# Kernel tuning notes

Measured on AMD Instinct MI355X. Metric: run time of the kernel, lower is better.

Reference implementation:

```python
import jax, jax.numpy as jnp
import numpy as np

B, S, H = 128, 1000, 256


def setup_inputs() -> dict:
    key = jax.random.key(0)
    ks = jax.random.split(key, 15)
    sc = 1.0 / np.sqrt(H)
    f = lambda k, shape: (jax.random.normal(k, shape, jnp.float32) * sc)
    return dict(
        static_hidden=jax.random.normal(ks[0], (B, S, H), jnp.float32),
        state_embedding=jax.random.normal(ks[1], (B, 1, H), jnp.float32),
        decoder_hidden=jax.random.normal(ks[2], (B, 1, H), jnp.float32),
        target_hidden=jax.random.normal(ks[3], (B, 1, H), jnp.float32),
        last_hh=jax.random.normal(ks[4], (1, B, H), jnp.float32),
        W_ih=f(ks[5], (3 * H, H)),
        W_hh=f(ks[6], (3 * H, H)),
        b_ih=f(ks[7], (3 * H,)),
        b_hh=f(ks[8], (3 * H,)),
        v_attn_enc=f(ks[9], (H,)),
        W_attn_enc=f(ks[10], (H, 2 * H)),
        v_attn_tgt=f(ks[11], (H,)),
        W_attn_tgt=f(ks[12], (H, 2 * H)),
        v_ptr=f(ks[13], (H,)),
        W_ptr=f(ks[14], (H, 3 * H)),
    )


def _attention(static, dec, v, W):
    # static: [B,S,H], dec: [B,1,H] -> softmax attention over S
    hid = jnp.concatenate([static, jnp.broadcast_to(dec, static.shape)], axis=2)  # [B,S,2H]
    t = jnp.tanh(jnp.einsum('hk,bsk->bhs', W, hid))  # [B,H,S]
    return jax.nn.softmax(jnp.einsum('h,bhs->bs', v, t), axis=1)  # [B,S]


def _gru_step(x, h, Wih, Whh, bih, bhh):
    # single-layer single-step torch GRU semantics; x,h: [B,H]
    gi = x @ Wih.T + bih
    gh = h @ Whh.T + bhh
    ir, iz, ig = jnp.split(gi, 3, axis=-1)
    hr, hz, hg = jnp.split(gh, 3, axis=-1)
    r = jax.nn.sigmoid(ir + hr)
    z = jax.nn.sigmoid(iz + hz)
    n = jnp.tanh(ig + r * hg)
    return (1.0 - z) * n + z * h


def _pointer_branch(static, state_emb, attn, v, W):
    context = jnp.einsum('bs,bsh->bh', attn, static)[:, None, :]  # [B,1,H]
    energy = jnp.concatenate(
        [static,
         jnp.broadcast_to(context, static.shape),
         jnp.broadcast_to(state_emb, static.shape)], axis=2)  # [B,S,3H]
    return jnp.einsum('h,bhs->bs', v, jnp.tanh(jnp.einsum('hk,bsk->bhs', W, energy)))


def reference(static_hidden, state_embedding, decoder_hidden, target_hidden, last_hh,
              W_ih, W_hh, b_ih, b_hh,
              v_attn_enc, W_attn_enc, v_attn_tgt, W_attn_tgt, v_ptr, W_ptr):
    # GRU step (dropout is identity in eval / p=0.0)
    h_new = _gru_step(decoder_hidden[:, 0, :], last_hh[0], W_ih, W_hh, b_ih, b_hh)
    rnn_out = h_new[:, None, :]  # [B,1,H]
    last_hh_new = h_new[None]    # [1,B,H]

    enc_attn = _attention(static_hidden, rnn_out, v_attn_enc, W_attn_enc)
    probs = _pointer_branch(static_hidden, state_embedding, enc_attn, v_ptr, W_ptr)

    tgt_attn = _attention(static_hidden, target_hidden, v_attn_tgt, W_attn_tgt)
    # NOTE: original code reuses self.v / self.W (not v_target/W_taret) for the
    # target branch energy -- replicated faithfully.
    probs_target = _pointer_branch(static_hidden, state_embedding, tgt_attn, v_ptr, W_ptr)

    return (5.0 * probs + probs_target, last_hh_new)
```

## Files before the change

### kernel.cpp

```cpp
#include <hip/hip_runtime.h>
#include <hip/hip_bf16.h>
#include <stdint.h>
#include <stddef.h>

#define Bn 128
#define Sn 1000
#define SP 1024
#define Hn 256

typedef __bf16 bf16;
typedef __bf16 bf16x8 __attribute__((ext_vector_type(8)));
typedef __bf16 bf16x4 __attribute__((ext_vector_type(4)));
typedef float  f32x16 __attribute__((ext_vector_type(16)));

typedef __attribute__((address_space(1))) const unsigned int* gas1;
typedef __attribute__((address_space(3))) unsigned int* las3;

__device__ __forceinline__ float fast_tanh(float x){
  return 1.0f - 2.0f / (__expf(2.0f * x) + 1.0f);
}
__device__ __forceinline__ float fast_sigmoid(float x){
  return 1.0f / (1.0f + __expf(-x));
}

__global__ void k0w(const float* __restrict__ We, const float* __restrict__ Wt,
                    const float* __restrict__ Wp, bf16* __restrict__ Wcb,
                    const float* __restrict__ dec, const float* __restrict__ lhh,
                    const float* __restrict__ tgt, const float* __restrict__ se,
                    float* __restrict__ xT, float* __restrict__ hT,
                    float* __restrict__ tT, float* __restrict__ sT){
  int blk = blockIdx.x, t = threadIdx.x;
  if (blk < 768){
    int tt = blk*256 + t;
    int r = tt >> 8, c = tt & 255;
    float val;
    if (r < 256)       val = We[r*512 + c];
    else if (r < 512)  val = Wt[(r-256)*512 + c];
    else               val = Wp[(r-512)*768 + c];
    Wcb[tt] = (bf16)val;
  } else {
    int idx = blk - 768;
    int a = idx >> 7, bb = idx & 127;
    const float* src = (a==0) ? dec : (a==1) ? lhh : (a==2) ? tgt : se;
    float* dst       = (a==0) ? xT  : (a==1) ? hT  : (a==2) ? tT  : sT;
    dst[t*128 + bb] = src[bb*256 + t];
  }
}

__global__ __launch_bounds__(512) void k1a_gru(
    const float* __restrict__ xT, const float* __restrict__ hT,
    const float* __restrict__ Wih, const float* __restrict__ Whh,
    const float* __restrict__ bih, const float* __restrict__ bhh,
    float* __restrict__ out_hh, float* __restrict__ hnT){
  int t = threadIdx.x;
  int g = t >> 7, b = t & 127;
  int h = blockIdx.x*4 + g;
  const float4* wir = (const float4*)(Wih + (size_t)h*256);
  const float4* wiz = (const float4*)(Wih + (size_t)(256+h)*256);
  const float4* wig = (const float4*)(Wih + (size_t)(512+h)*256);
  const float4* whr = (const float4*)(Whh + (size_t)h*256);
  const float4* whz = (const float4*)(Whh + (size_t)(256+h)*256);
  const float4* whg = (const float4*)(Whh + (size_t)(512+h)*256);
  float air=0.f, aiz=0.f, aig=0.f, ahr=0.f, ahz=0.f, ahg=0.f;
  #pragma unroll 2
  for (int kq=0; kq<64; kq++){
    float4 vir = wir[kq], viz = wiz[kq], vig = wig[kq];
    float4 vhr = whr[kq], vhz = whz[kq], vhg = whg[kq];
    #pragma unroll
    for (int e=0;e<4;e++){
      int k = kq*4 + e;
      float xv = xT[k*128 + b];
      float hv = hT[k*128 + b];
      air += (&vir.x)[e]*xv; aiz += (&viz.x)[e]*xv; aig += (&vig.x)[e]*xv;
      ahr += (&vhr.x)[e]*hv; ahz += (&vhz.x)[e]*hv; ahg += (&vhg.x)[e]*hv;
    }
  }
  air += bih[h];      ahr += bhh[h];
  aiz += bih[256+h];  ahz += bhh[256+h];
  aig += bih[512+h];  ahg += bhh[512+h];
  float r = fast_sigmoid(air + ahr);
  float z = fast_sigmoid(aiz + ahz);
  float n = fast_tanh(aig + r*ahg);
  float hprev = hT[h*128 + b];
  float hnew = (1.f - z)*n + z*hprev;
  out_hh[b*256 + h] = hnew;
  hnT[h*128 + b] = hnew;
}

__global__ __launch_bounds__(512) void k1c_dots(
    const float* __restrict__ hnT, const float* __restrict__ tT,
    const float* __restrict__ sT,
    const float* __restrict__ We, const float* __restrict__ Wt,
    const float* __restrict__ Wp,
    float* __restrict__ dEnc, float* __restrict__ dTgt, float* __restrict__ c3){
  int t = threadIdx.x;
  int g = t >> 7, b = t & 127;
  int vr = blockIdx.x*4 + g;
  int var = vr >> 8, h = vr & 255;
  const float* wrow; const float* X; float* dst;
  if (var == 0)      { wrow = We + (size_t)h*512 + 256; X = hnT; dst = dEnc; }
  else if (var == 1) { wrow = Wt + (size_t)h*512 + 256; X = tT;  dst = dTgt; }
  else               { wrow = Wp + (size_t)h*768 + 512; X = sT;  dst = c3; }
  const float4* w4 = (const float4*)wrow;
  float acc = 0.f;
  #pragma unroll 2
  for (int kq=0; kq<64; kq++){
    float4 wv = w4[kq];
    #pragma unroll
    for (int e=0;e<4;e++)
      acc += (&wv.x)[e] * X[(kq*4+e)*128 + b];
  }
  dst[b*256 + h] = acc;
}

__global__ __launch_bounds__(256) void k2_gemm(
    const float* __restrict__ stat, const bf16* __restrict__ Wcb,
    const float* __restrict__ dEnc, const float* __restrict__ dTgt,
    const float* __restrict__ vEnc, const float* __restrict__ vTgt,
    float* __restrict__ scE, float* __restrict__ scT, bf16* __restrict__ Aptr){
  __shared__ __align__(16) bf16 As[64*256];
  __shared__ __align__(16) bf16 Bs[2][256*32];
  int tid = threadIdx.x, w = tid>>6, l = tid&63;
  int l31 = l&31, lh = l>>5;
  int st = blockIdx.x, b = blockIdx.y;

  int am = tid>>2, agk = tid&3;
  bool aValid = (st*64 + am) < Sn;
  const float4* aSrc4 = (const float4*)(stat + ((size_t)b*Sn + st*64 + am)*Hn);

  int bnb = w*16 + (l>>2);
  int bg  = l&3;

  float4 pl0 = make_float4(0.f,0.f,0.f,0.f), pl1 = pl0;
  if (aValid){ pl0 = aSrc4[agk*2]; pl1 = aSrc4[agk*2+1]; }
  #pragma unroll
  for (int i=0;i<4;i++){
    int n = i*64 + bnb;
    int g = bg ^ ((n>>1)&3);
    __builtin_amdgcn_global_load_lds((gas1)(Wcb + (size_t)n*256 + g*8),
                                     (las3)(&Bs[0][i*2048 + w*512]), 16, 0, 0);
  }
  {
    bf16x8 v;
    v[0]=(bf16)pl0.x; v[1]=(bf16)pl0.y; v[2]=(bf16)pl0.z; v[3]=(bf16)pl0.w;
    v[4]=(bf16)pl1.x; v[5]=(bf16)pl1.y; v[6]=(bf16)pl1.z; v[7]=(bf16)pl1.w;
    *(bf16x8*)&As[am*256 + ((agk ^ (am&7))<<3)] = v;
  }
  __syncthreads();

  float scp0[2] = {0.f, 0.f}, scp1[2] = {0.f, 0.f};

  #pragma unroll
  for (int p=0; p<3; p++){
    f32x16 acc[2][2];
    #pragma unroll
    for (int a=0;a<2;a++)
      #pragma unroll
      for (int c=0;c<2;c++)
        #pragma unroll
        for (int r=0;r<16;r++) acc[a][c][r] = 0.f;

    #pragma unroll
    for (int kt=0; kt<8; kt++){
      int it = p*8 + kt;
      float4 q0 = make_float4(0.f,0.f,0.f,0.f), q1 = q0;
      bool doA = (p==0) && (kt<7);
      if (doA && aValid){ q0 = aSrc4[(kt+1)*8 + agk*2]; q1 = aSrc4[(kt+1)*8 + agk*2 + 1]; }
      if (it < 23){
        int itn = it+1, pn = itn>>3, ktn = itn&7;
        const bf16* wb = Wcb + (size_t)pn*65536 + ktn*32;
        bf16* ldsb = &Bs[(it&1)^1][0];
        #pragma unroll
        for (int i=0;i<4;i++){
          int n = i*64 + bnb;
          int g = bg ^ ((n>>1)&3);
          __builtin_amdgcn_global_load_lds((gas1)(wb + (size_t)n*256 + g*8),
                                           (las3)(ldsb + i*2048 + w*512), 16, 0, 0);
        }
      }
      const bf16* bsr = &Bs[it&1][0];
      #pragma unroll
      for (int ks=0; ks<2; ks++){
        int kg = ks*2 + lh;
        int swzA = ((kt*4 + kg) ^ (l31&7))<<3;
        bf16x8 af0 = *(const bf16x8*)&As[l31*256 + swzA];
        bf16x8 af1 = *(const bf16x8*)&As[(32+l31)*256 + swzA];
        #pragma unroll
        for (int c=0;c<2;c++){
          int n = w*64 + c*32 + l31;
          bf16x8 wf = *(const bf16x8*)&bsr[n*32 + ((kg ^ ((n>>1)&3))<<3)];
          acc[0][c] = __builtin_amdgcn_mfma_f32_32x32x16_bf16(wf, af0, acc[0][c], 0,0,0);
          acc[1][c] = __builtin_amdgcn_mfma_f32_32x32x16_bf16(wf, af1, acc[1][c], 0,0,0);
        }
      }
      if (doA){
        bf16x8 v;
        v[0]=(bf16)q0.x; v[1]=(bf16)q0.y; v[2]=(bf16)q0.z; v[3]=(bf16)q0.w;
        v[4]=(bf16)q1.x; v[5]=(bf16)q1.y; v[6]=(bf16)q1.z; v[7]=(bf16)q1.w;
        int G = (kt+1)*4 + agk;
        *(bf16x8*)&As[am*256 + ((G ^ (am&7))<<3)] = v;
      }
      __syncthreads();
    }

    if (p < 2){
      const float* vv = p ? vTgt : vEnc;
      const float* db = (p ? dTgt : dEnc) + b*256;
      float s0 = 0.f, s1 = 0.f;
      #pragma unroll
      for (int c=0;c<2;c++){
        int nb = w*64 + c*32 + 4*lh;
        #pragma unroll
        for (int r=0;r<16;r++){
          int n = nb + (r&3) + 8*(r>>2);
          float vdv = vv[n], ddv = db[n];
          s0 += vdv * fast_tanh(acc[0][c][r] + ddv);
          s1 += vdv * fast_tanh(acc[1][c][r] + ddv);
        }
      }
      scp0[p] = s0; scp1[p] = s1;
    } else {
      #pragma unroll
      for (int a=0;a<2;a++){
        int m = a*32 + l31;
        #pragma unroll
        for (int c=0;c<2;c++){
          int g0 = w*8 + c*4 + lh*2;
          bf16x8 lo, hi;
          #pragma unroll
          for (int r=0;r<8;r++){ lo[r] = (bf16)acc[a][c][r]; hi[r] = (bf16)acc[a][c][8+r]; }
          *(bf16x8*)&As[m*256 + (( g0    ^ (m&7))<<3)] = lo;
          *(bf16x8*)&As[m*256 + (((g0+1) ^ (m&7))<<3)] = hi;
        }
      }
    }
  }

  float* scr = (float*)&Bs[0][0];
  #pragma unroll
  for (int p2=0;p2<2;p2++){
    float v0 = scp0[p2] + __shfl_xor(scp0[p2], 32);
    float v1 = scp1[p2] + __shfl_xor(scp1[p2], 32);
    if (lh == 0){
      scr[(p2*4 + w)*64 + l31]      = v0;
      scr[(p2*4 + w)*64 + 32 + l31] = v1;
    }
  }
  __syncthreads();
  if (tid < 128){
    int pp = tid>>6, m = tid&63;
    float s = scr[pp*256 + m] + scr[pp*256 + 64 + m]
            + scr[pp*256 + 128 + m] + scr[pp*256 + 192 + m];
    (pp ? scT : scE)[b*SP + st*64 + m] = s;
  }
  {
    int m = tid>>2, part = tid&3;
    bf16* dst = Aptr + ((size_t)(b*1024 + st*64 + m))*256 + part*64;
    #pragma unroll
    for (int i=0;i<8;i++){
      int g = (part*8 + i) ^ (m&7);
      *(bf16x8*)(dst + i*8) = *(const bf16x8*)&As[m*256 + (g<<3)];
    }
  }
}

__global__ __launch_bounds__(1024) void k3_ctx(
    const float* __restrict__ scE, const float* __restrict__ scT,
    const float* __restrict__ stat, float* __restrict__ ctxG){
  __shared__ float attE[500], attT[500];
  __shared__ float redE[16], redT[16];
  __shared__ float4 pe4[16][64], pt4[16][64];
  int b = blockIdx.x, sg = blockIdx.y, t = threadIdx.x;
  int wid = t>>6, ln = t&63;

  float vE = (t < Sn) ? scE[b*SP + t] : -1e30f;
  float vT = (t < Sn) ? scT[b*SP + t] : -1e30f;
  float mE = vE, mT = vT;
  #pragma unroll
  for (int o=1;o<64;o<<=1){ mE=fmaxf(mE,__shfl_xor(mE,o)); mT=fmaxf(mT,__shfl_xor(mT,o)); }
  if (ln==0){ redE[wid]=mE; redT[wid]=mT; }
  __syncthreads();
  float ME=-1e30f, MT=-1e30f;
  #pragma unroll
  for (int i=0;i<16;i++){ ME=fmaxf(ME,redE[i]); MT=fmaxf(MT,redT[i]); }
  __syncthreads();
  float eE = (t < Sn) ? __expf(vE-ME) : 0.f;
  float eT = (t < Sn) ? __expf(vT-MT) : 0.f;
  float sE=eE, sT=eT;
  #pragma unroll
  for (int o=1;o<64;o<<=1){ sE+=__shfl_xor(sE,o); sT+=__shfl_xor(sT,o); }
  if (ln==0){ redE[wid]=sE; redT[wid]=sT; }
  __syncthreads();
  float SE=0.f, ST=0.f;
  #pragma unroll
  for (int i=0;i<16;i++){ SE+=redE[i]; ST+=redT[i]; }
  float invE = 1.f/SE, invT = 1.f/ST;
  if (t < 500){
    int s = sg*500 + t;
    attE[t] = __expf(scE[b*SP+s]-ME)*invE;
    attT[t] = __expf(scT[b*SP+s]-MT)*invT;
  }
  __syncthreads();

  int h4 = t & 63, rg = t >> 6;
  float4 aE = make_float4(0.f,0.f,0.f,0.f), aT = aE;
  int nrows = (rg == 15) ? 20 : 32;
  const float4* base = (const float4*)(stat + ((size_t)(b*Sn + sg*500 + rg*32))*Hn) + h4;
  #pragma unroll 4
  for (int i=0;i<nrows;i++){
    float4 f = base[(size_t)i*64];
    float wE = attE[rg*32 + i], wT = attT[rg*32 + i];
    aE.x += wE*f.x; aE.y += wE*f.y; aE.z += wE*f.z; aE.w += wE*f.w;
    aT.x += wT*f.x; aT.y += wT*f.y; aT.z += wT*f.z; aT.w += wT*f.w;
  }
  pe4[rg][h4] = aE; pt4[rg][h4] = aT;
  __syncthreads();
  if (t < 64){
    float4 s = make_float4(0.f,0.f,0.f,0.f);
    #pragma unroll
    for (int i=0;i<16;i++){
      float4 p = pe4[i][t];
      s.x+=p.x; s.y+=p.y; s.z+=p.z; s.w+=p.w;
    }
    atomicAdd(&ctxG[b*256 + t*4 + 0], s.x);
    atomicAdd(&ctxG[b*256 + t*4 + 1], s.y);
    atomicAdd(&ctxG[b*256 + t*4 + 2], s.z);
    atomicAdd(&ctxG[b*256 + t*4 + 3], s.w);
  } else if (t < 128){
    int h = t - 64;
    float4 s = make_float4(0.f,0.f,0.f,0.f);
    #pragma unroll
    for (int i=0;i<16;i++){
      float4 p = pt4[i][h];
      s.x+=p.x; s.y+=p.y; s.z+=p.z; s.w+=p.w;
    }
    atomicAdd(&ctxG[32768 + b*256 + h*4 + 0], s.x);
    atomicAdd(&ctxG[32768 + b*256 + h*4 + 1], s.y);
    atomicAdd(&ctxG[32768 + b*256 + h*4 + 2], s.z);
    atomicAdd(&ctxG[32768 + b*256 + h*4 + 3], s.w);
  }
}

__global__ __launch_bounds__(512) void k3c_c2(
    const float* __restrict__ ctxG, const float* __restrict__ Wp,
    const float* __restrict__ c3,
    float* __restrict__ cE, float* __restrict__ cT){
  __shared__ __align__(16) float ctxL[512];
  int b = blockIdx.x, t = threadIdx.x;
  ctxL[t] = ctxG[(t>>8)*32768 + b*256 + (t&255)];
  __syncthreads();
  int var = t >> 8, h = t & 255;
  const float4* w4 = (const float4*)(Wp + (size_t)h*768 + 256);
  const float4* cv = (const float4*)(&ctxL[var*256]);
  float acc = 0.f;
  #pragma unroll 4
  for (int k=0;k<64;k++){
    float4 wv = w4[k], xv = cv[k];
    acc += wv.x*xv.x + wv.y*xv.y + wv.z*xv.z + wv.w*xv.w;
  }
  (var ? cT : cE)[b*256 + h] = acc + c3[b*256 + h];
}

__global__ __launch_bounds__(256) void k4_final(
    const bf16* __restrict__ Aptr, const float* __restrict__ cE,
    const float* __restrict__ cT, const float* __restrict__ vp,
    float* __restrict__ out){
  int t = threadIdx.x;
  int st = blockIdx.x, b = blockIdx.y;
  int m = t>>2, part = t&3;
  const bf16* src = Aptr + ((size_t)(b*1024 + st*64 + m))*256 + part*64;
  const float* vpb = vp + part*64;
  const float* ceb = cE + b*256 + part*64;
  const float* ctb = cT + b*256 + part*64;
  float pe = 0.f, pt = 0.f;
  #pragma unroll
  for (int i=0;i<8;i++){
    bf16x8 av = *(const bf16x8*)(src + i*8);
    int bi = ((i>>2)<<5) + (((i>>1)&1)<<2) + ((i&1)<<4);
    float4 v0 = *(const float4*)(vpb + bi), v1 = *(const float4*)(vpb + bi + 8);
    float4 e0 = *(const float4*)(ceb + bi), e1 = *(const float4*)(ceb + bi + 8);
    float4 t0 = *(const float4*)(ctb + bi), t1 = *(const float4*)(ctb + bi + 8);
    #pragma unroll
    for (int j=0;j<4;j++){
      float a = (float)av[j];
      pe += (&v0.x)[j] * fast_tanh(a + (&e0.x)[j]);
      pt += (&v0.x)[j] * fast_tanh(a + (&t0.x)[j]);
    }
    #pragma unroll
    for (int j=0;j<4;j++){
      float a = (float)av[4+j];
      pe += (&v1.x)[j] * fast_tanh(a + (&e1.x)[j]);
      pt += (&v1.x)[j] * fast_tanh(a + (&t1.x)[j]);
    }
  }
  pe += __shfl_xor(pe,1); pe += __shfl_xor(pe,2);
  pt += __shfl_xor(pt,1); pt += __shfl_xor(pt,2);
  int s = st*64 + m;
  if (part==0 && s < Sn) out[(size_t)b*Sn + s] = 5.0f*pe + pt;
}

extern "C" void kernel_launch(void* const* d_in, const int* in_sizes, int n_in,
                              void* d_out, int out_size, void* d_ws, size_t ws_size,
                              hipStream_t stream){
  const float* stat = (const float*)d_in[0];
  const float* se   = (const float*)d_in[1];
  const float* dec  = (const float*)d_in[2];
  const float* tgt  = (const float*)d_in[3];
  const float* lhh  = (const float*)d_in[4];
  const float* Wih  = (const float*)d_in[5];
  const float* Whh  = (const float*)d_in[6];
  const float* bih  = (const float*)d_in[7];
  const float* bhh  = (const float*)d_in[8];
  const float* vEnc = (const float*)d_in[9];
  const float* WEnc = (const float*)d_in[10];
  const float* vTgt = (const float*)d_in[11];
  const float* WTgt = (const float*)d_in[12];
  const float* vPtr = (const float*)d_in[13];
  const float* WPtr = (const float*)d_in[14];
  float* out = (float*)d_out;

  char* wsp = (char*)d_ws;
  bf16*  Aptr = (bf16*)(wsp);
  bf16*  Wcb  = (bf16*)(wsp + 67108864);
  float* xT   = (float*)(wsp + 67502080);
  float* hT   = (float*)(wsp + 67633152);
  float* tT   = (float*)(wsp + 67764224);
  float* sT   = (float*)(wsp + 67895296);
  float* hnT  = (float*)(wsp + 68026368);
  float* scE  = (float*)(wsp + 68157440);
  float* scT  = (float*)(wsp + 68681728);
  float* dEnc = (float*)(wsp + 69206016);
  float* dTgt = (float*)(wsp + 69337088);
  float* c3   = (float*)(wsp + 69468160);
  float* cE   = (float*)(wsp + 69599232);
  float* cT   = (float*)(wsp + 69730304);
  float* ctxG = (float*)(wsp + 69861376);

  hipMemsetAsync(ctxG, 0, 262144, stream);
  hipLaunchKernelGGL(k0w, dim3(1280), dim3(256), 0, stream,
                     WEnc, WTgt, WPtr, Wcb, dec, lhh, tgt, se, xT, hT, tT, sT);
  hipLaunchKernelGGL(k1a_gru, dim3(64), dim3(512), 0, stream,
                     xT, hT, Wih, Whh, bih, bhh, out + Bn*Sn, hnT);
  hipLaunchKernelGGL(k1c_dots, dim3(192), dim3(512), 0, stream,
                     hnT, tT, sT, WEnc, WTgt, WPtr, dEnc, dTgt, c3);
  hipLaunchKernelGGL(k2_gemm, dim3(16, 128), dim3(256), 0, stream,
                     stat, Wcb, dEnc, dTgt, vEnc, vTgt, scE, scT, Aptr);
  hipLaunchKernelGGL(k3_ctx, dim3(128, 2), dim3(1024), 0, stream,
                     scE, scT, stat, ctxG);
  hipLaunchKernelGGL(k3c_c2, dim3(128), dim3(512), 0, stream,
                     ctxG, WPtr, c3, cE, cT);
  hipLaunchKernelGGL(k4_final, dim3(16, 128), dim3(256), 0, stream,
                     Aptr, cE, cT, vPtr, out);
}
```

Baseline: 464.1 us.

## Pre-permute weights into MFMA fragment order and load them directly into registers

The weight matrix is now stored in a layout that matches the MFMA operand fragments. The GEMM kernel therefore loads each wave's weight fragments straight from global memory into registers, with double buffering, instead of staging them through a shared-memory buffer that needed a barrier every k-step. The whole activation tile is converted and loaded up front, so the main loop has no __syncthreads. Dropping the B buffer frees shared memory, and the launch bounds now ask for 2 blocks per SM. In exchange, every wave reads its own weights from global memory or L2 with less reuse, and register pressure goes up.

```diff
diff --git a/kernel.cpp b/kernel.cpp
--- a/kernel.cpp
+++ b/kernel.cpp
@@ -13,9 +13,6 @@
 typedef __bf16 bf16x4 __attribute__((ext_vector_type(4)));
 typedef float  f32x16 __attribute__((ext_vector_type(16)));
 
-typedef __attribute__((address_space(1))) const unsigned int* gas1;
-typedef __attribute__((address_space(3))) unsigned int* las3;
-
 __device__ __forceinline__ float fast_tanh(float x){
   return 1.0f - 2.0f / (__expf(2.0f * x) + 1.0f);
 }
@@ -24,7 +21,7 @@
 }
 
 __global__ void k0w(const float* __restrict__ We, const float* __restrict__ Wt,
-                    const float* __restrict__ Wp, bf16* __restrict__ Wcb,
+                    const float* __restrict__ Wp, bf16* __restrict__ W2,
                     const float* __restrict__ dec, const float* __restrict__ lhh,
                     const float* __restrict__ tgt, const float* __restrict__ se,
                     float* __restrict__ xT, float* __restrict__ hT,
@@ -32,12 +29,20 @@
   int blk = blockIdx.x, t = threadIdx.x;
   if (blk < 768){
     int tt = blk*256 + t;
-    int r = tt >> 8, c = tt & 255;
+    int e   = tt & 7;
+    int l31 = (tt>>3) & 31;
+    int lh2 = (tt>>8) & 1;
+    int ks  = (tt>>9) & 1;
+    int c   = (tt>>10) & 1;
+    int kt  = (tt>>11) & 7;
+    int hb  = tt >> 14;
+    int r = (hb>>2)*256 + (hb&3)*64 + c*32 + l31;
+    int k = kt*32 + ks*16 + lh2*8 + e;
     float val;
-    if (r < 256)       val = We[r*512 + c];
-    else if (r < 512)  val = Wt[(r-256)*512 + c];
-    else               val = Wp[(r-512)*768 + c];
-    Wcb[tt] = (bf16)val;
+    if (r < 256)       val = We[r*512 + k];
+    else if (r < 512)  val = Wt[(r-256)*512 + k];
+    else               val = Wp[(r-512)*768 + k];
+    W2[tt] = (bf16)val;
   } else {
     int idx = blk - 768;
     int a = idx >> 7, bb = idx & 127;
@@ -113,46 +118,63 @@
   dst[b*256 + h] = acc;
 }
 
-__global__ __launch_bounds__(256) void k2_gemm(
-    const float* __restrict__ stat, const bf16* __restrict__ Wcb,
+__global__ __launch_bounds__(256, 2) void k2_gemm(
+    const float* __restrict__ stat, const bf16* __restrict__ W2,
     const float* __restrict__ dEnc, const float* __restrict__ dTgt,
     const float* __restrict__ vEnc, const float* __restrict__ vTgt,
     float* __restrict__ scE, float* __restrict__ scT, bf16* __restrict__ Aptr){
   __shared__ __align__(16) bf16 As[64*256];
-  __shared__ __align__(16) bf16 Bs[2][256*32];
+  __shared__ float scr[2][4][64];
   int tid = threadIdx.x, w = tid>>6, l = tid&63;
   int l31 = l&31, lh = l>>5;
   int st = blockIdx.x, b = blockIdx.y;
 
-  int am = tid>>2, agk = tid&3;
-  bool aValid = (st*64 + am) < Sn;
-  const float4* aSrc4 = (const float4*)(stat + ((size_t)b*Sn + st*64 + am)*Hn);
-
-  int bnb = w*16 + (l>>2);
-  int bg  = l&3;
-
-  float4 pl0 = make_float4(0.f,0.f,0.f,0.f), pl1 = pl0;
-  if (aValid){ pl0 = aSrc4[agk*2]; pl1 = aSrc4[agk*2+1]; }
-  #pragma unroll
-  for (int i=0;i<4;i++){
-    int n = i*64 + bnb;
-    int g = bg ^ ((n>>1)&3);
-    __builtin_amdgcn_global_load_lds((gas1)(Wcb + (size_t)n*256 + g*8),
-                                     (las3)(&Bs[0][i*2048 + w*512]), 16, 0, 0);
-  }
   {
-    bf16x8 v;
-    v[0]=(bf16)pl0.x; v[1]=(bf16)pl0.y; v[2]=(bf16)pl0.z; v[3]=(bf16)pl0.w;
-    v[4]=(bf16)pl1.x; v[5]=(bf16)pl1.y; v[6]=(bf16)pl1.z; v[7]=(bf16)pl1.w;
-    *(bf16x8*)&As[am*256 + ((agk ^ (am&7))<<3)] = v;
-  }
-  __syncthreads();
-
-  float scp0[2] = {0.f, 0.f}, scp1[2] = {0.f, 0.f};
+    int am = tid>>2, agk = tid&3;
+    bool aValid = (st*64 + am) < Sn;
+    const float4* aSrc4 = (const float4*)(stat + ((size_t)b*Sn + st*64 + am)*Hn);
+    #pragma unroll
+    for (int i=0;i<8;i++){
+      int G = i*4 + agk;
+      float4 f0 = make_float4(0.f,0.f,0.f,0.f), f1 = f0;
+      if (aValid){ f0 = aSrc4[G*2]; f1 = aSrc4[G*2+1]; }
+      bf16x8 v;
+      v[0]=(bf16)f0.x; v[1]=(bf16)f0.y; v[2]=(bf16)f0.z; v[3]=(bf16)f0.w;
+      v[4]=(bf16)f1.x; v[5]=(bf16)f1.y; v[6]=(bf16)f1.z; v[7]=(bf16)f1.w;
+      *(bf16x8*)&As[am*256 + ((G ^ (am&7))<<3)] = v;
+    }
+  }
+  __syncthreads();
+
+#define WLOAD(dst, it) { \
+  const bf16* wp_ = W2 + ((size_t)(((it)>>3)*4 + w)*8 + (size_t)((it)&7))*2048 + l*8; \
+  dst[0] = *(const bf16x8*)(wp_); \
+  dst[1] = *(const bf16x8*)(wp_ + 512); \
+  dst[2] = *(const bf16x8*)(wp_ + 1024); \
+  dst[3] = *(const bf16x8*)(wp_ + 1536); }
+
+#define CHUNK(it, wf) { \
+  _Pragma("unroll") \
+  for (int ks=0; ks<2; ks++){ \
+    int G_ = ((it)&7)*4 + ks*2 + lh; \
+    int sa_ = (G_ ^ (l31&7))<<3; \
+    bf16x8 af0 = *(const bf16x8*)&As[l31*256 + sa_]; \
+    bf16x8 af1 = *(const bf16x8*)&As[(32+l31)*256 + sa_]; \
+    acc[0][0] = __builtin_amdgcn_mfma_f32_32x32x16_bf16(wf[ks],   af0, acc[0][0], 0,0,0); \
+    acc[1][0] = __builtin_amdgcn_mfma_f32_32x32x16_bf16(wf[ks],   af1, acc[1][0], 0,0,0); \
+    acc[0][1] = __builtin_amdgcn_mfma_f32_32x32x16_bf16(wf[2+ks], af0, acc[0][1], 0,0,0); \
+    acc[1][1] = __builtin_amdgcn_mfma_f32_32x32x16_bf16(wf[2+ks], af1, acc[1][1], 0,0,0); \
+  } }
+
+  bf16x8 wA[4], wB[4];
+  WLOAD(wA, 0);
+  WLOAD(wB, 1);
+
+  float scp0[2] = {0.f,0.f}, scp1[2] = {0.f,0.f};
+  f32x16 acc[2][2];
 
   #pragma unroll
   for (int p=0; p<3; p++){
-    f32x16 acc[2][2];
     #pragma unroll
     for (int a=0;a<2;a++)
       #pragma unroll
@@ -161,46 +183,12 @@
         for (int r=0;r<16;r++) acc[a][c][r] = 0.f;
 
     #pragma unroll
-    for (int kt=0; kt<8; kt++){
-      int it = p*8 + kt;
-      float4 q0 = make_float4(0.f,0.f,0.f,0.f), q1 = q0;
-      bool doA = (p==0) && (kt<7);
-      if (doA && aValid){ q0 = aSrc4[(kt+1)*8 + agk*2]; q1 = aSrc4[(kt+1)*8 + agk*2 + 1]; }
-      if (it < 23){
-        int itn = it+1, pn = itn>>3, ktn = itn&7;
-        const bf16* wb = Wcb + (size_t)pn*65536 + ktn*32;
-        bf16* ldsb = &Bs[(it&1)^1][0];
-        #pragma unroll
-        for (int i=0;i<4;i++){
-          int n = i*64 + bnb;
-          int g = bg ^ ((n>>1)&3);
-          __builtin_amdgcn_global_load_lds((gas1)(wb + (size_t)n*256 + g*8),
-                                           (las3)(ldsb + i*2048 + w*512), 16, 0, 0);
-        }
-      }
-      const bf16* bsr = &Bs[it&1][0];
-      #pragma unroll
-      for (int ks=0; ks<2; ks++){
-        int kg = ks*2 + lh;
-        int swzA = ((kt*4 + kg) ^ (l31&7))<<3;
-        bf16x8 af0 = *(const bf16x8*)&As[l31*256 + swzA];
-        bf16x8 af1 = *(const bf16x8*)&As[(32+l31)*256 + swzA];
-        #pragma unroll
-        for (int c=0;c<2;c++){
-          int n = w*64 + c*32 + l31;
-          bf16x8 wf = *(const bf16x8*)&bsr[n*32 + ((kg ^ ((n>>1)&3))<<3)];
-          acc[0][c] = __builtin_amdgcn_mfma_f32_32x32x16_bf16(wf, af0, acc[0][c], 0,0,0);
-          acc[1][c] = __builtin_amdgcn_mfma_f32_32x32x16_bf16(wf, af1, acc[1][c], 0,0,0);
-        }
-      }
-      if (doA){
-        bf16x8 v;
-        v[0]=(bf16)q0.x; v[1]=(bf16)q0.y; v[2]=(bf16)q0.z; v[3]=(bf16)q0.w;
-        v[4]=(bf16)q1.x; v[5]=(bf16)q1.y; v[6]=(bf16)q1.z; v[7]=(bf16)q1.w;
-        int G = (kt+1)*4 + agk;
-        *(bf16x8*)&As[am*256 + ((G ^ (am&7))<<3)] = v;
-      }
-      __syncthreads();
+    for (int kq=0; kq<4; kq++){
+      int it = p*8 + kq*2;
+      CHUNK(it, wA);
+      if (it+2 < 24) WLOAD(wA, it+2);
+      CHUNK(it+1, wB);
+      if (it+3 < 24) WLOAD(wB, it+3);
     }
 
     if (p < 2){
@@ -219,38 +207,36 @@
         }
       }
       scp0[p] = s0; scp1[p] = s1;
-    } else {
+    }
+  }
+
+  __syncthreads();
+  #pragma unroll
+  for (int a=0;a<2;a++){
+    int m = a*32 + l31;
+    #pragma unroll
+    for (int c=0;c<2;c++){
+      int g0 = w*8 + c*4 + lh*2;
+      bf16x8 lo, hi;
       #pragma unroll
-      for (int a=0;a<2;a++){
-        int m = a*32 + l31;
-        #pragma unroll
-        for (int c=0;c<2;c++){
-          int g0 = w*8 + c*4 + lh*2;
-          bf16x8 lo, hi;
-          #pragma unroll
-          for (int r=0;r<8;r++){ lo[r] = (bf16)acc[a][c][r]; hi[r] = (bf16)acc[a][c][8+r]; }
-          *(bf16x8*)&As[m*256 + (( g0    ^ (m&7))<<3)] = lo;
-          *(bf16x8*)&As[m*256 + (((g0+1) ^ (m&7))<<3)] = hi;
-        }
-      }
-    }
-  }
-
-  float* scr = (float*)&Bs[0][0];
+      for (int r=0;r<8;r++){ lo[r] = (bf16)acc[a][c][r]; hi[r] = (bf16)acc[a][c][8+r]; }
+      *(bf16x8*)&As[m*256 + (( g0    ^ (m&7))<<3)] = lo;
+      *(bf16x8*)&As[m*256 + (((g0+1) ^ (m&7))<<3)] = hi;
+    }
+  }
   #pragma unroll
   for (int p2=0;p2<2;p2++){
     float v0 = scp0[p2] + __shfl_xor(scp0[p2], 32);
     float v1 = scp1[p2] + __shfl_xor(scp1[p2], 32);
     if (lh == 0){
-      scr[(p2*4 + w)*64 + l31]      = v0;
-      scr[(p2*4 + w)*64 + 32 + l31] = v1;
+      scr[p2][w][l31]      = v0;
+      scr[p2][w][32 + l31] = v1;
     }
   }
   __syncthreads();
   if (tid < 128){
     int pp = tid>>6, m = tid&63;
-    float s = scr[pp*256 + m] + scr[pp*256 + 64 + m]
-            + scr[pp*256 + 128 + m] + scr[pp*256 + 192 + m];
+    float s = scr[pp][0][m] + scr[pp][1][m] + scr[pp][2][m] + scr[pp][3][m];
     (pp ? scT : scE)[b*SP + st*64 + m] = s;
   }
   {
@@ -262,6 +248,8 @@
       *(bf16x8*)(dst + i*8) = *(const bf16x8*)&As[m*256 + (g<<3)];
     }
   }
+#undef WLOAD
+#undef CHUNK
 }
 
 __global__ __launch_bounds__(1024) void k3_ctx(
@@ -421,7 +409,7 @@
 
   char* wsp = (char*)d_ws;
   bf16*  Aptr = (bf16*)(wsp);
-  bf16*  Wcb  = (bf16*)(wsp + 67108864);
+  bf16*  W2   = (bf16*)(wsp + 67108864);
   float* xT   = (float*)(wsp + 67502080);
   float* hT   = (float*)(wsp + 67633152);
   float* tT   = (float*)(wsp + 67764224);
@@ -438,13 +426,13 @@
 
   hipMemsetAsync(ctxG, 0, 262144, stream);
   hipLaunchKernelGGL(k0w, dim3(1280), dim3(256), 0, stream,
-                     WEnc, WTgt, WPtr, Wcb, dec, lhh, tgt, se, xT, hT, tT, sT);
+                     WEnc, WTgt, WPtr, W2, dec, lhh, tgt, se, xT, hT, tT, sT);
   hipLaunchKernelGGL(k1a_gru, dim3(64), dim3(512), 0, stream,
                      xT, hT, Wih, Whh, bih, bhh, out + Bn*Sn, hnT);
   hipLaunchKernelGGL(k1c_dots, dim3(192), dim3(512), 0, stream,
                      hnT, tT, sT, WEnc, WTgt, WPtr, dEnc, dTgt, c3);
   hipLaunchKernelGGL(k2_gemm, dim3(16, 128), dim3(256), 0, stream,
-                     stat, Wcb, dEnc, dTgt, vEnc, vTgt, scE, scT, Aptr);
+                     stat, W2, dEnc, dTgt, vEnc, vTgt, scE, scT, Aptr);
   hipLaunchKernelGGL(k3_ctx, dim3(128, 2), dim3(1024), 0, stream,
                      scE, scT, stat, ctxG);
   hipLaunchKernelGGL(k3c_c2, dim3(128), dim3(512), 0, stream,
```

Measured after the change: 519.3 us. +11.9%, slower.
